# Kernel tuning notes

Measured on AMD Instinct MI355X. Metric: run time of the kernel, lower is better.

Reference implementation:

```python
import jax, jax.numpy as jnp
import numpy as np

B, T, C = 2, 2048, 2048
N_HEAD = 16
HS = C // N_HEAD
D_LATENT = C // 2


def setup_inputs() -> dict:
    key = jax.random.key(0)
    ks = jax.random.split(key, 7)
    s = 0.02
    return {
        "x": jax.random.normal(ks[0], (B, T, C), dtype=jnp.float32),
        "Wq": jax.random.normal(ks[1], (C, C), dtype=jnp.float32) * s,
        "Wc": jax.random.normal(ks[2], (C, D_LATENT), dtype=jnp.float32) * s,
        "Wk": jax.random.normal(ks[3], (D_LATENT, C), dtype=jnp.float32) * s,
        "Wv": jax.random.normal(ks[4], (D_LATENT, C), dtype=jnp.float32) * s,
        "Wo": jax.random.normal(ks[5], (C, C), dtype=jnp.float32) * s,
        "bo": jnp.zeros((C,), dtype=jnp.float32),
    }


def reference(x, Wq, Wc, Wk, Wv, Wo, bo):
    b, t, c = x.shape
    # projections (torch Linear without bias, weights stored as (in, out))
    q = x @ Wq                    # (B,T,C)
    c_latent = x @ Wc             # (B,T,d_latent)
    k = c_latent @ Wk             # (B,T,C)
    v = c_latent @ Wv             # (B,T,C)
    # split heads -> (B,H,T,hs)
    q = q.reshape(b, t, N_HEAD, HS).transpose(0, 2, 1, 3)
    k = k.reshape(b, t, N_HEAD, HS).transpose(0, 2, 1, 3)
    v = v.reshape(b, t, N_HEAD, HS).transpose(0, 2, 1, 3)
    scale = 1.0 / jnp.sqrt(jnp.asarray(HS, dtype=x.dtype))
    scores = jnp.einsum('bhqd,bhkd->bhqk', q, k) * scale
    causal = jnp.tril(jnp.ones((t, t), dtype=bool))
    scores = jnp.where(causal, scores, jnp.finfo(scores.dtype).min)
    attn = jax.nn.softmax(scores, axis=-1)
    y = jnp.einsum('bhqk,bhkd->bhqd', attn, v)      # (B,H,T,hs)
    y = y.transpose(0, 2, 1, 3).reshape(b, t, c)
    return y @ Wo + bo
```

## Files before the change

### kernel.cpp

```cpp
#include <hip/hip_runtime.h>
#include <hip/hip_bf16.h>
#include <math.h>

typedef __hip_bfloat16 bf16;
typedef __attribute__((ext_vector_type(8))) short bf16x8;
typedef __attribute__((ext_vector_type(4))) float f32x4;

#define B_  2
#define T_  2048
#define C_  2048
#define H_  16
#define HS_ 128
#define DL_ 1024
#define M_  (B_ * T_)
#define NT64_ 32

__device__ inline void lds16(const bf16* g, bf16* l) {
    __builtin_amdgcn_global_load_lds(
        (const __attribute__((address_space(1))) void*)g,
        (__attribute__((address_space(3))) void*)l, 16, 0, 0);
}

__global__ __launch_bounds__(256) void cast_bf16_k(
    const float* __restrict__ in, bf16* __restrict__ out)
{
    const size_t i = ((size_t)blockIdx.x * 256 + threadIdx.x) * 8;
    const float4 a = *(const float4*)(in + i);
    const float4 b = *(const float4*)(in + i + 4);
    bf16 o[8];
    o[0] = __float2bfloat16(a.x); o[1] = __float2bfloat16(a.y);
    o[2] = __float2bfloat16(a.z); o[3] = __float2bfloat16(a.w);
    o[4] = __float2bfloat16(b.x); o[5] = __float2bfloat16(b.y);
    o[6] = __float2bfloat16(b.z); o[7] = __float2bfloat16(b.w);
    *(uint4*)(out + i) = *(const uint4*)o;
}

__global__ __launch_bounds__(256) void transpose_cast5(
    const float* __restrict__ s0, const float* __restrict__ s1,
    const float* __restrict__ s2, const float* __restrict__ s3,
    const float* __restrict__ s4,
    bf16* __restrict__ d0, bf16* __restrict__ d1, bf16* __restrict__ d2,
    bf16* __restrict__ d3, bf16* __restrict__ d4)
{
    const float* in; bf16* out; int R, Cc;
    switch (blockIdx.z) {
        case 0: in = s0; out = d0; R = C_;  Cc = C_;  break;
        case 1: in = s1; out = d1; R = C_;  Cc = DL_; break;
        case 2: in = s2; out = d2; R = DL_; Cc = C_;  break;
        case 3: in = s3; out = d3; R = DL_; Cc = C_;  break;
        default: in = s4; out = d4; R = C_; Cc = C_;  break;
    }
    const int bx = blockIdx.x * 32, by = blockIdx.y * 32;
    if (bx >= Cc || by >= R) return;
    __shared__ float t[32][33];
    const int tx = threadIdx.x & 31, ty = threadIdx.x >> 5;
#pragma unroll
    for (int i = 0; i < 32; i += 8)
        t[ty + i][tx] = in[(size_t)(by + ty + i) * Cc + bx + tx];
    __syncthreads();
#pragma unroll
    for (int i = 0; i < 32; i += 8)
        out[(size_t)(bx + ty + i) * R + by + tx] = __float2bfloat16(t[tx][ty + i]);
}

#define GEMM_CORE(A_, Bt_, Kdim)                                               \
    __shared__ __align__(16) bf16 As[128 * 64];                                \
    __shared__ __align__(16) bf16 Bs[128 * 64];                                \
    const int tid  = threadIdx.x;                                              \
    const int lane = tid & 63;                                                 \
    const int wave = tid >> 6;                                                 \
    const int wm = wave >> 1, wn = wave & 1;                                   \
    const int quad = lane >> 4, l16 = lane & 15;                               \
    const int sw8 = (l16 >> 1) & 7;                                            \
    f32x4 acc[4][4];                                                           \
    _Pragma("unroll")                                                          \
    for (int i = 0; i < 4; i++)                                                \
        _Pragma("unroll")                                                      \
        for (int j = 0; j < 4; j++) acc[i][j] = (f32x4){0.f, 0.f, 0.f, 0.f};   \
    const int srow = tid >> 3;                                                 \
    const int ssl  = (((tid & 7) ^ ((srow >> 1) & 7)) * 8);                    \
    const bf16* Ap = (A_)  + (size_t)(m0 + srow) * (Kdim) + ssl;               \
    const bf16* Bp = (Bt_) + (size_t)(n0 + srow) * (Kdim) + ssl;               \
    const size_t rstr = (size_t)32 * (Kdim);                                   \
    for (int k0 = 0; k0 < (Kdim); k0 += 64) {                                  \
        if (k0) __syncthreads();                                               \
        _Pragma("unroll")                                                      \
        for (int ii = 0; ii < 4; ii++) {                                       \
            lds16(Ap + ii * rstr + k0, As + ii * 2048 + tid * 8);              \
            lds16(Bp + ii * rstr + k0, Bs + ii * 2048 + tid * 8);              \
        }                                                                      \
        __syncthreads();                                                       \
        _Pragma("unroll")                                                      \
        for (int w = 0; w < 2; w++) {                                          \
            bf16x8 af[4], bfr[4];                                              \
            _Pragma("unroll")                                                  \
            for (int mi = 0; mi < 4; mi++)                                     \
                af[mi] = *(const bf16x8*)&As[(wm * 64 + mi * 16 + l16) * 64 +  \
                                            (((w << 2) | quad) ^ sw8) * 8];    \
            _Pragma("unroll")                                                  \
            for (int ni = 0; ni < 4; ni++)                                     \
                bfr[ni] = *(const bf16x8*)&Bs[(wn * 64 + ni * 16 + l16) * 64 + \
                                              (((w << 2) | quad) ^ sw8) * 8];  \
            _Pragma("unroll")                                                  \
            for (int mi = 0; mi < 4; mi++)                                     \
                _Pragma("unroll")                                              \
                for (int ni = 0; ni < 4; ni++)                                 \
                    acc[mi][ni] = __builtin_amdgcn_mfma_f32_16x16x32_bf16(     \
                        af[mi], bfr[ni], acc[mi][ni], 0, 0, 0);                \
        }                                                                      \
    }

__global__ __launch_bounds__(256) void gemm_bt_mfma(
    const bf16* __restrict__ A, const bf16* __restrict__ Bt,
    bf16* __restrict__ Cbf, float* __restrict__ Cf32,
    const float* __restrict__ bias, int M, int N, int K)
{
    const int m0 = blockIdx.y * 128, n0 = blockIdx.x * 128;
    GEMM_CORE(A, Bt, K)
#pragma unroll
    for (int mi = 0; mi < 4; mi++) {
#pragma unroll
        for (int ni = 0; ni < 4; ni++) {
            const int col = n0 + wn * 64 + ni * 16 + l16;
#pragma unroll
            for (int r = 0; r < 4; r++) {
                const int row = m0 + wm * 64 + mi * 16 + quad * 4 + r;
                if (Cf32)
                    Cf32[(size_t)row * N + col] = acc[mi][ni][r] + bias[col];
                else
                    Cbf[(size_t)row * N + col] = __float2bfloat16(acc[mi][ni][r]);
            }
        }
    }
}

__global__ __launch_bounds__(256) void gemm_qc_fused(
    const bf16* __restrict__ A, const bf16* __restrict__ Bt,
    bf16* __restrict__ Cq, bf16* __restrict__ Cc, int M, int K)
{
    const int m0 = blockIdx.y * 128, n0 = blockIdx.x * 128;
    GEMM_CORE(A, Bt, K)
    const bool is_q = (n0 < C_);
    const float scl = is_q ? 0.08838834764831845f : 1.0f;
    bf16* dst = is_q ? Cq : Cc;
    const int ld   = is_q ? C_ : DL_;
    const int coff = is_q ? 0 : C_;
#pragma unroll
    for (int mi = 0; mi < 4; mi++) {
#pragma unroll
        for (int ni = 0; ni < 4; ni++) {
            const int col = n0 - coff + wn * 64 + ni * 16 + l16;
#pragma unroll
            for (int r = 0; r < 4; r++) {
                const int row = m0 + wm * 64 + mi * 16 + quad * 4 + r;
                dst[(size_t)row * ld + col] = __float2bfloat16(acc[mi][ni][r] * scl);
            }
        }
    }
}

__global__ __launch_bounds__(256) void gemm_kv_fused(
    const bf16* __restrict__ clat, const bf16* __restrict__ Wk_t,
    const bf16* __restrict__ Wv_t, bf16* __restrict__ kk, bf16* __restrict__ vt)
{
    const int bid = blockIdx.x;
    const bf16 *A, *Bt; bf16* dst; int N, m0, n0;
    if (bid < 512) { A = clat; Bt = Wk_t; dst = kk; N = C_;
                     m0 = (bid >> 4) * 128; n0 = (bid & 15) * 128; }
    else           { const int t = bid - 512;
                     A = Wv_t; Bt = clat; dst = vt; N = M_;
                     m0 = (t >> 5) * 128; n0 = (t & 31) * 128; }
    GEMM_CORE(A, Bt, DL_)
#pragma unroll
    for (int mi = 0; mi < 4; mi++) {
#pragma unroll
        for (int ni = 0; ni < 4; ni++) {
            const int col = n0 + wn * 64 + ni * 16 + l16;
#pragma unroll
            for (int r = 0; r < 4; r++) {
                const int row = m0 + wm * 64 + mi * 16 + quad * 4 + r;
                dst[(size_t)row * N + col] = __float2bfloat16(acc[mi][ni][r]);
            }
        }
    }
}

__global__ __launch_bounds__(256) void flash_dual(
    const bf16* __restrict__ Q, const bf16* __restrict__ K,
    const bf16* __restrict__ Vt, bf16* __restrict__ Y)
{
    __shared__ __align__(16) bf16 Ks[2][4][64][32];
    __shared__ __align__(16) bf16 Vs[2][2][128][32];
    __shared__ __align__(16) bf16 Ps[4][16][72];
    const int tid  = threadIdx.x;
    const int lane = tid & 63, wv = tid >> 6;
    const int quad = lane >> 4, l16 = lane & 15;
    const int sw = (l16 >> 1) & 3;
    const int bid = blockIdx.x;
    const int bh = (bid & 7) * 4 + ((bid >> 3) & 3);
    const int pa = bid >> 5;
    const int b = bh >> 4, h = bh & 15;
    const int qA0 = pa * 64, qB0 = (NT64_ - 1 - pa) * 64;
    const int jA = pa + 1;
    const int jB = NT64_ - pa;

    const int sr  = tid >> 2;
    const int ssl = ((tid & 3) ^ ((sr >> 1) & 3)) * 8;

    bf16x8 qfA[4], qfB[4];
    {
        const size_t rA = (size_t)(b * T_ + qA0 + wv * 16 + l16) * C_ + h * HS_;
        const size_t rB = (size_t)(b * T_ + qB0 + wv * 16 + l16) * C_ + h * HS_;
#pragma unroll
        for (int c = 0; c < 4; c++) {
            qfA[c] = *(const bf16x8*)(Q + rA + c * 32 + quad * 8);
            qfB[c] = *(const bf16x8*)(Q + rB + c * 32 + quad * 8);
        }
    }

    f32x4 oA[8], oB[8];
#pragma unroll
    for (int dt = 0; dt < 8; dt++) {
        oA[dt] = (f32x4){0.f, 0.f, 0.f, 0.f};
        oB[dt] = (f32x4){0.f, 0.f, 0.f, 0.f};
    }
    float lA[4] = {0.f, 0.f, 0.f, 0.f}, lB[4] = {0.f, 0.f, 0.f, 0.f};

    auto stage = [&](int j, int buf) {
        const int kv0 = j * 64;
#pragma unroll
        for (int kc = 0; kc < 4; kc++)
            lds16(K + (size_t)(b * T_ + kv0 + sr) * C_ + h * HS_ + kc * 32 + ssl,
                  &Ks[buf][kc][0][0] + tid * 8);
#pragma unroll
        for (int vc = 0; vc < 2; vc++)
#pragma unroll
            for (int hf = 0; hf < 2; hf++)
                lds16(Vt + (size_t)(h * HS_ + hf * 64 + sr) * M_ + b * T_ + kv0 + vc * 32 + ssl,
                      &Vs[buf][vc][hf * 64][0] + tid * 8);
    };

    auto tile = [&](int buf, int kv0, int q0, const bf16x8* qf, f32x4* oacc, float* l_s) {
        const int rowbase = q0 + wv * 16;
        if (kv0 > rowbase + 15) return;
        f32x4 sacc[4];
#pragma unroll
        for (int nt = 0; nt < 4; nt++) sacc[nt] = (f32x4){0.f, 0.f, 0.f, 0.f};
#pragma unroll
        for (int c = 0; c < 4; c++) {
            bf16x8 kf[4];
#pragma unroll
            for (int nt = 0; nt < 4; nt++)
                kf[nt] = *(const bf16x8*)&Ks[buf][c][nt * 16 + l16][(quad ^ sw) * 8];
#pragma unroll
            for (int nt = 0; nt < 4; nt++)
                sacc[nt] = __builtin_amdgcn_mfma_f32_16x16x32_bf16(qf[c], kf[nt], sacc[nt], 0, 0, 0);
        }
        float p[4][4];
        if (kv0 + 63 > rowbase) {
#pragma unroll
            for (int nt = 0; nt < 4; nt++)
#pragma unroll
                for (int r = 0; r < 4; r++) {
                    const int col = kv0 + nt * 16 + l16;
                    const int row = rowbase + quad * 4 + r;
                    p[nt][r] = (col <= row) ? __expf(sacc[nt][r]) : 0.f;
                }
        } else {
#pragma unroll
            for (int nt = 0; nt < 4; nt++)
#pragma unroll
                for (int r = 0; r < 4; r++)
                    p[nt][r] = __expf(sacc[nt][r]);
        }
#pragma unroll
        for (int r = 0; r < 4; r++)
            l_s[r] += p[0][r] + p[1][r] + p[2][r] + p[3][r];
#pragma unroll
        for (int nt = 0; nt < 4; nt++)
#pragma unroll
            for (int r = 0; r < 4; r++)
                Ps[wv][quad * 4 + r][nt * 16 + l16] = __float2bfloat16(p[nt][r]);
        const bf16x8 pa0 = *(const bf16x8*)&Ps[wv][l16][quad * 8];
        const bf16x8 pa1 = *(const bf16x8*)&Ps[wv][l16][32 + quad * 8];
#pragma unroll
        for (int dt = 0; dt < 8; dt++) {
            const bf16x8 vf0 = *(const bf16x8*)&Vs[buf][0][dt * 16 + l16][(quad ^ sw) * 8];
            const bf16x8 vf1 = *(const bf16x8*)&Vs[buf][1][dt * 16 + l16][(quad ^ sw) * 8];
            oacc[dt] = __builtin_amdgcn_mfma_f32_16x16x32_bf16(pa0, vf0, oacc[dt], 0, 0, 0);
            oacc[dt] = __builtin_amdgcn_mfma_f32_16x16x32_bf16(pa1, vf1, oacc[dt], 0, 0, 0);
        }
    };

    stage(0, 0);
    for (int j = 0; j < jB; j++) {
        const int kv0 = j * 64;
        if (j + 1 < jB) {
            stage(j + 1, (j + 1) & 1);
            __asm__ __volatile__("s_waitcnt vmcnt(8)" ::: "memory");
        } else {
            __asm__ __volatile__("s_waitcnt vmcnt(0)" ::: "memory");
        }
        __builtin_amdgcn_s_barrier();
        tile(j & 1, kv0, qB0, qfB, oB, lB);
        if (j < jA) tile(j & 1, kv0, qA0, qfA, oA, lA);
        __asm__ __volatile__("s_waitcnt lgkmcnt(0)" ::: "memory");
        __builtin_amdgcn_s_barrier();
    }

    auto finish = [&](int q0, f32x4* oacc, float* l_s) {
        float inv[4];
#pragma unroll
        for (int r = 0; r < 4; r++) {
            float l = l_s[r];
            l += __shfl_xor(l, 1);
            l += __shfl_xor(l, 2);
            l += __shfl_xor(l, 4);
            l += __shfl_xor(l, 8);
            inv[r] = 1.f / l;
        }
        const int rowbase = q0 + wv * 16;
#pragma unroll
        for (int dt = 0; dt < 8; dt++)
#pragma unroll
            for (int r = 0; r < 4; r++)
                Y[(size_t)(b * T_ + rowbase + quad * 4 + r) * C_ + h * HS_ + dt * 16 + l16] =
                    __float2bfloat16(oacc[dt][r] * inv[r]);
    };
    finish(qA0, oA, lA);
    finish(qB0, oB, lB);
}

extern "C" void kernel_launch(void* const* d_in, const int* in_sizes, int n_in,
                              void* d_out, int out_size, void* d_ws, size_t ws_size,
                              hipStream_t stream) {
    const float* x  = (const float*)d_in[0];
    const float* Wq = (const float*)d_in[1];
    const float* Wc = (const float*)d_in[2];
    const float* Wk = (const float*)d_in[3];
    const float* Wv = (const float*)d_in[4];
    const float* Wo = (const float*)d_in[5];
    const float* bo = (const float*)d_in[6];
    float* out = (float*)d_out;

    bf16* ws   = (bf16*)d_ws;
    bf16* x_bf = ws;
    bf16* Wq_t = x_bf + (size_t)M_ * C_;
    bf16* Wc_t = Wq_t + (size_t)C_ * C_;
    bf16* Wk_t = Wc_t + (size_t)DL_ * C_;
    bf16* Wv_t = Wk_t + (size_t)C_ * DL_;
    bf16* Wo_t = Wv_t + (size_t)C_ * DL_;
    bf16* q    = Wo_t + (size_t)C_ * C_;
    bf16* clat = q    + (size_t)M_ * C_;
    bf16* kk   = clat + (size_t)M_ * DL_;
    bf16* vt   = kk   + (size_t)M_ * C_;
    bf16* y    = vt   + (size_t)C_ * M_;

    const dim3 blk(256);

    cast_bf16_k<<<dim3((M_ * C_) / (256 * 8)), blk, 0, stream>>>(x, x_bf);
    transpose_cast5<<<dim3(C_ / 32, C_ / 32, 5), blk, 0, stream>>>(
        Wq, Wc, Wk, Wv, Wo, Wq_t, Wc_t, Wk_t, Wv_t, Wo_t);

    gemm_qc_fused<<<dim3((C_ + DL_) / 128, M_ / 128), blk, 0, stream>>>(
        x_bf, Wq_t, q, clat, M_, C_);
    gemm_kv_fused<<<dim3(1024), blk, 0, stream>>>(clat, Wk_t, Wv_t, kk, vt);

    flash_dual<<<dim3((NT64_ / 2) * H_ * B_), blk, 0, stream>>>(q, kk, vt, y);

    gemm_bt_mfma<<<dim3(C_ / 128, M_ / 128), blk, 0, stream>>>(
        y, Wo_t, nullptr, out, bo, M_, C_, C_);
}
```

Measured before the change: 365.8 us.

## Split flash loop into dual-tile and single-tile phases with interleaved MFMAs

```diff
diff --git a/kernel.cpp b/kernel.cpp
--- a/kernel.cpp
+++ b/kernel.cpp
@@ -185,7 +185,7 @@
     }
 }
 
-__global__ __launch_bounds__(256) void flash_dual(
+__global__ __launch_bounds__(256, 2) void flash_dual(
     const bf16* __restrict__ Q, const bf16* __restrict__ K,
     const bf16* __restrict__ Vt, bf16* __restrict__ Y)
 {
@@ -225,27 +225,64 @@
         oB[dt] = (f32x4){0.f, 0.f, 0.f, 0.f};
     }
     float lA[4] = {0.f, 0.f, 0.f, 0.f}, lB[4] = {0.f, 0.f, 0.f, 0.f};
-
-    auto stage = [&](int j, int buf) {
+    const int rbA = qA0 + wv * 16, rbB = qB0 + wv * 16;
+
+    auto stage = [&](int j, int sbuf) {
         const int kv0 = j * 64;
 #pragma unroll
         for (int kc = 0; kc < 4; kc++)
             lds16(K + (size_t)(b * T_ + kv0 + sr) * C_ + h * HS_ + kc * 32 + ssl,
-                  &Ks[buf][kc][0][0] + tid * 8);
+                  &Ks[sbuf][kc][0][0] + tid * 8);
 #pragma unroll
         for (int vc = 0; vc < 2; vc++)
 #pragma unroll
             for (int hf = 0; hf < 2; hf++)
                 lds16(Vt + (size_t)(h * HS_ + hf * 64 + sr) * M_ + b * T_ + kv0 + vc * 32 + ssl,
-                      &Vs[buf][vc][hf * 64][0] + tid * 8);
+                      &Vs[sbuf][vc][hf * 64][0] + tid * 8);
     };
 
-    auto tile = [&](int buf, int kv0, int q0, const bf16x8* qf, f32x4* oacc, float* l_s) {
-        const int rowbase = q0 + wv * 16;
-        if (kv0 > rowbase + 15) return;
-        f32x4 sacc[4];
-#pragma unroll
-        for (int nt = 0; nt < 4; nt++) sacc[nt] = (f32x4){0.f, 0.f, 0.f, 0.f};
+    auto sm_half = [&](const f32x4* s, int nt0, float* l_s, bool diag,
+                       int kv0, int rowbase) {
+        float p[2][4];
+#pragma unroll
+        for (int t = 0; t < 2; t++)
+#pragma unroll
+            for (int r = 0; r < 4; r++) {
+                const int nt = nt0 + t;
+                float e = __expf(s[nt][r]);
+                if (diag) {
+                    const int col = kv0 + nt * 16 + l16;
+                    const int row = rowbase + quad * 4 + r;
+                    if (col > row) e = 0.f;
+                }
+                p[t][r] = e;
+            }
+#pragma unroll
+        for (int r = 0; r < 4; r++) l_s[r] += p[0][r] + p[1][r];
+#pragma unroll
+        for (int t = 0; t < 2; t++)
+#pragma unroll
+            for (int r = 0; r < 4; r++)
+                Ps[wv][quad * 4 + r][(nt0 + t) * 16 + l16] = __float2bfloat16(p[t][r]);
+        return *(const bf16x8*)&Ps[wv][l16][nt0 * 16 + quad * 8];
+    };
+
+    stage(0, 0);
+
+    for (int j = 0; j < jA; j++) {
+        const int kv0 = j * 64;
+        stage(j + 1, (j + 1) & 1);
+        __asm__ __volatile__("s_waitcnt vmcnt(8)" ::: "memory");
+        __builtin_amdgcn_s_barrier();
+        const int buf = j & 1;
+
+        f32x4 sA[4], sB[4];
+#pragma unroll
+        for (int nt = 0; nt < 4; nt++) {
+            sA[nt] = (f32x4){0.f, 0.f, 0.f, 0.f};
+            sB[nt] = (f32x4){0.f, 0.f, 0.f, 0.f};
+        }
+        __builtin_amdgcn_s_setprio(1);
 #pragma unroll
         for (int c = 0; c < 4; c++) {
             bf16x8 kf[4];
@@ -253,47 +290,38 @@
             for (int nt = 0; nt < 4; nt++)
                 kf[nt] = *(const bf16x8*)&Ks[buf][c][nt * 16 + l16][(quad ^ sw) * 8];
 #pragma unroll
-            for (int nt = 0; nt < 4; nt++)
-                sacc[nt] = __builtin_amdgcn_mfma_f32_16x16x32_bf16(qf[c], kf[nt], sacc[nt], 0, 0, 0);
-        }
-        float p[4][4];
-        if (kv0 + 63 > rowbase) {
-#pragma unroll
-            for (int nt = 0; nt < 4; nt++)
-#pragma unroll
-                for (int r = 0; r < 4; r++) {
-                    const int col = kv0 + nt * 16 + l16;
-                    const int row = rowbase + quad * 4 + r;
-                    p[nt][r] = (col <= row) ? __expf(sacc[nt][r]) : 0.f;
-                }
-        } else {
-#pragma unroll
-            for (int nt = 0; nt < 4; nt++)
-#pragma unroll
-                for (int r = 0; r < 4; r++)
-                    p[nt][r] = __expf(sacc[nt][r]);
-        }
-#pragma unroll
-        for (int r = 0; r < 4; r++)
-            l_s[r] += p[0][r] + p[1][r] + p[2][r] + p[3][r];
-#pragma unroll
-        for (int nt = 0; nt < 4; nt++)
-#pragma unroll
-            for (int r = 0; r < 4; r++)
-                Ps[wv][quad * 4 + r][nt * 16 + l16] = __float2bfloat16(p[nt][r]);
-        const bf16x8 pa0 = *(const bf16x8*)&Ps[wv][l16][quad * 8];
-        const bf16x8 pa1 = *(const bf16x8*)&Ps[wv][l16][32 + quad * 8];
+            for (int nt = 0; nt < 4; nt++) {
+                sB[nt] = __builtin_amdgcn_mfma_f32_16x16x32_bf16(qfB[c], kf[nt], sB[nt], 0, 0, 0);
+                sA[nt] = __builtin_amdgcn_mfma_f32_16x16x32_bf16(qfA[c], kf[nt], sA[nt], 0, 0, 0);
+            }
+        }
+        __builtin_amdgcn_s_setprio(0);
+
+        const bool dA = (j == jA - 1);
+        const bf16x8 pB0 = sm_half(sB, 0, lB, false, kv0, rbB);
+        const bf16x8 pB1 = sm_half(sB, 2, lB, false, kv0, rbB);
+        const bf16x8 pA0 = sm_half(sA, 0, lA, dA, kv0, rbA);
+        const bf16x8 pA1 = sm_half(sA, 2, lA, dA, kv0, rbA);
+
+        __builtin_amdgcn_s_setprio(1);
 #pragma unroll
         for (int dt = 0; dt < 8; dt++) {
             const bf16x8 vf0 = *(const bf16x8*)&Vs[buf][0][dt * 16 + l16][(quad ^ sw) * 8];
+            oB[dt] = __builtin_amdgcn_mfma_f32_16x16x32_bf16(pB0, vf0, oB[dt], 0, 0, 0);
+            oA[dt] = __builtin_amdgcn_mfma_f32_16x16x32_bf16(pA0, vf0, oA[dt], 0, 0, 0);
+        }
+#pragma unroll
+        for (int dt = 0; dt < 8; dt++) {
             const bf16x8 vf1 = *(const bf16x8*)&Vs[buf][1][dt * 16 + l16][(quad ^ sw) * 8];
-            oacc[dt] = __builtin_amdgcn_mfma_f32_16x16x32_bf16(pa0, vf0, oacc[dt], 0, 0, 0);
-            oacc[dt] = __builtin_amdgcn_mfma_f32_16x16x32_bf16(pa1, vf1, oacc[dt], 0, 0, 0);
-        }
-    };
-
-    stage(0, 0);
-    for (int j = 0; j < jB; j++) {
+            oB[dt] = __builtin_amdgcn_mfma_f32_16x16x32_bf16(pB1, vf1, oB[dt], 0, 0, 0);
+            oA[dt] = __builtin_amdgcn_mfma_f32_16x16x32_bf16(pA1, vf1, oA[dt], 0, 0, 0);
+        }
+        __builtin_amdgcn_s_setprio(0);
+        __asm__ __volatile__("s_waitcnt lgkmcnt(0)" ::: "memory");
+        __builtin_amdgcn_s_barrier();
+    }
+
+    for (int j = jA; j < jB; j++) {
         const int kv0 = j * 64;
         if (j + 1 < jB) {
             stage(j + 1, (j + 1) & 1);
@@ -302,8 +330,40 @@
             __asm__ __volatile__("s_waitcnt vmcnt(0)" ::: "memory");
         }
         __builtin_amdgcn_s_barrier();
-        tile(j & 1, kv0, qB0, qfB, oB, lB);
-        if (j < jA) tile(j & 1, kv0, qA0, qfA, oA, lA);
+        const int buf = j & 1;
+
+        f32x4 sB[4];
+#pragma unroll
+        for (int nt = 0; nt < 4; nt++) sB[nt] = (f32x4){0.f, 0.f, 0.f, 0.f};
+        __builtin_amdgcn_s_setprio(1);
+#pragma unroll
+        for (int c = 0; c < 4; c++) {
+            bf16x8 kf[4];
+#pragma unroll
+            for (int nt = 0; nt < 4; nt++)
+                kf[nt] = *(const bf16x8*)&Ks[buf][c][nt * 16 + l16][(quad ^ sw) * 8];
+#pragma unroll
+            for (int nt = 0; nt < 4; nt++)
+                sB[nt] = __builtin_amdgcn_mfma_f32_16x16x32_bf16(qfB[c], kf[nt], sB[nt], 0, 0, 0);
+        }
+        __builtin_amdgcn_s_setprio(0);
+
+        const bool dB = (j == jB - 1);
+        const bf16x8 pB0 = sm_half(sB, 0, lB, dB, kv0, rbB);
+        const bf16x8 pB1 = sm_half(sB, 2, lB, dB, kv0, rbB);
+
+        __builtin_amdgcn_s_setprio(1);
+#pragma unroll
+        for (int dt = 0; dt < 8; dt++) {
+            const bf16x8 vf0 = *(const bf16x8*)&Vs[buf][0][dt * 16 + l16][(quad ^ sw) * 8];
+            oB[dt] = __builtin_amdgcn_mfma_f32_16x16x32_bf16(pB0, vf0, oB[dt], 0, 0, 0);
+        }
+#pragma unroll
+        for (int dt = 0; dt < 8; dt++) {
+            const bf16x8 vf1 = *(const bf16x8*)&Vs[buf][1][dt * 16 + l16][(quad ^ sw) * 8];
+            oB[dt] = __builtin_amdgcn_mfma_f32_16x16x32_bf16(pB1, vf1, oB[dt], 0, 0, 0);
+        }
+        __builtin_amdgcn_s_setprio(0);
         __asm__ __volatile__("s_waitcnt lgkmcnt(0)" ::: "memory");
         __builtin_amdgcn_s_barrier();
     }
```

Measured after the change: 357.0 us. -2.4%, faster.
